# Optimization experiments

Hardware: AMD Instinct MI355X
Metric: run time of the kernel (lower is better)

## Reference

```python
import jax, jax.numpy as jnp
import numpy as np

NHEAD = 16


def setup_inputs() -> dict:
    key = jax.random.key(0)
    ks = jax.random.split(key, 8)
    B, T, C = 2, 1024, 2048
    H, D = NHEAD, C // NHEAD
    P = 1024  # past kv length
    s = 0.02
    return {
        "x": jax.random.normal(ks[0], (B, T, C), jnp.float32),
        "past_k": jax.random.normal(ks[1], (B, H, P, D), jnp.float32),
        "past_v": jax.random.normal(ks[2], (B, H, P, D), jnp.float32),
        "Wk": jax.random.normal(ks[3], (C, C), jnp.float32) * s,
        "Wq": jax.random.normal(ks[4], (C, C), jnp.float32) * s,
        "Wv": jax.random.normal(ks[5], (C, C), jnp.float32) * s,
        "Wp": jax.random.normal(ks[6], (C, C), jnp.float32) * s,
        "bp": jax.random.normal(ks[7], (C,), jnp.float32) * s,
    }


def reference(x, past_k, past_v, Wk, Wq, Wv, Wp, bp):
    B, T, C = x.shape
    H = NHEAD
    D = C // H
    # nn.Linear(W): y = x @ W.T ; split into heads -> [B,H,T,D]
    def proj_heads(W):
        return (x @ W.T).reshape(B, T, H, D).transpose(0, 2, 1, 3)
    q = proj_heads(Wq)
    k_new = proj_heads(Wk)
    v_new = proj_heads(Wv)
    k = jnp.concatenate([past_k, k_new], axis=2)  # [B,H,P+T,D]
    v = jnp.concatenate([past_v, v_new], axis=2)
    past_len = past_k.shape[2]
    total_len = past_len + T
    # causal mask: new-query row i attends to absolute position j <= past_len + i
    q_pos = past_len + jnp.arange(T)[:, None]        # [T,1]
    k_pos = jnp.arange(total_len)[None, :]           # [1,total]
    mask = k_pos <= q_pos                            # [T,total]
    att = jnp.einsum("bhqd,bhkd->bhqk", q, k) * (1.0 / np.sqrt(D).astype(np.float32))
    att = jnp.where(mask[None, None], att, jnp.float32(-jnp.inf))
    att = jax.nn.softmax(att, axis=-1)
    out = jnp.einsum("bhqk,bhkd->bhqd", att, v)
    out = out.transpose(0, 2, 1, 3).reshape(B, T, C)
    out = out @ Wp.T + bp
    return out, k, v
```

## Files before the change

### kernel.cpp

```cpp
#include <hip/hip_runtime.h>
#include <stdint.h>

#define B_ 2
#define T_ 1024
#define C_ 2048
#define H_ 16
#define D_ 128
#define P_ 1024
#define L_ 2048
#define M_ 2048

typedef unsigned short u16;
typedef __attribute__((ext_vector_type(8))) short short8;
typedef __attribute__((ext_vector_type(4))) float f32x4;
typedef __attribute__((ext_vector_type(8))) u16 u16x8;
typedef __attribute__((ext_vector_type(4))) u16 u16x4;

__device__ __forceinline__ u16 f2bf(float x) {
    union { float f; uint32_t u; } c; c.f = x;
    uint32_t u = c.u;
    return (u16)((u + 0x7fffu + ((u >> 16) & 1u)) >> 16);
}

__device__ __forceinline__ void gload_lds16(const void* g, void* l) {
    typedef __attribute__((address_space(1))) const void gvoid;
    typedef __attribute__((address_space(3))) void lvoid;
    __builtin_amdgcn_global_load_lds((gvoid*)g, (lvoid*)l, 16, 0, 0);
}

__global__ __launch_bounds__(256) void convert_bf16_kernel(
        const float* __restrict__ in, u16* __restrict__ out) {
    int i = blockIdx.x * 256 + threadIdx.x;
    const float4* p = (const float4*)in;
    float4 a = p[i * 2], b = p[i * 2 + 1];
    ((u16x8*)out)[i] = u16x8{f2bf(a.x), f2bf(a.y), f2bf(a.z), f2bf(a.w),
                             f2bf(b.x), f2bf(b.y), f2bf(b.z), f2bf(b.w)};
}

__global__ __launch_bounds__(256) void copy_past_kernel(
        const float4* __restrict__ pk, const float4* __restrict__ pv,
        float4* __restrict__ kdst, float4* __restrict__ vdst,
        u16x4* __restrict__ kb) {
    int i = blockIdx.x * 256 + threadIdx.x;
    int bh = i >> 15;
    int rest = i & 32767;
    size_t dst = (size_t)bh * (L_ * D_ / 4) + rest;
    float4 k4 = pk[i], v4 = pv[i];
    kdst[dst] = k4;
    vdst[dst] = v4;
    kb[dst] = u16x4{f2bf(k4.x), f2bf(k4.y), f2bf(k4.z), f2bf(k4.w)};
}

__global__ __launch_bounds__(256) void vT_past_kernel(
        const float* __restrict__ pv, u16* __restrict__ vbT) {
    __shared__ float s[64][65];
    const int tid = threadIdx.x;
    const int bh = blockIdx.x >> 5;
    const int tile = blockIdx.x & 31;
    const int k0 = (tile >> 1) * 64;
    const int d0 = (tile & 1) * 64;
    const float* src = pv + ((size_t)bh * P_ + k0) * D_ + d0;
    {
        int r = tid >> 2, c0 = (tid & 3) * 16;
#pragma unroll
        for (int u = 0; u < 4; ++u) {
            float4 f = *(const float4*)(src + (size_t)r * D_ + c0 + u * 4);
            s[r][c0 + u * 4 + 0] = f.x; s[r][c0 + u * 4 + 1] = f.y;
            s[r][c0 + u * 4 + 2] = f.z; s[r][c0 + u * 4 + 3] = f.w;
        }
    }
    __syncthreads();
    int d = tid >> 2, ck = (tid & 3) * 16;
    u16* dst = vbT + ((size_t)bh * D_ + d0 + d) * L_ + k0 + ck;
    u16x8 o0, o1;
#pragma unroll
    for (int j = 0; j < 8; ++j) o0[j] = f2bf(s[ck + j][d]);
#pragma unroll
    for (int j = 0; j < 8; ++j) o1[j] = f2bf(s[ck + 8 + j][d]);
    *(u16x8*)dst = o0;
    *(u16x8*)(dst + 8) = o1;
}

template <int MODE>
__global__ __launch_bounds__(256) void gemm128(
        const u16* __restrict__ A, const u16* __restrict__ Bw,
        float* __restrict__ outf, u16* __restrict__ outb,
        const float* __restrict__ bias) {
    __shared__ u16 As[128 * 32];
    __shared__ u16 Bs[128 * 32];
    const int tid  = threadIdx.x;
    const int wave = tid >> 6;
    const int lane = tid & 63;
    const int m0 = blockIdx.y * 128;
    const int n0 = blockIdx.x * 128;

    f32x4 acc[4][4];
#pragma unroll
    for (int i = 0; i < 4; ++i)
#pragma unroll
        for (int j = 0; j < 4; ++j) acc[i][j] = f32x4{0.f, 0.f, 0.f, 0.f};

    const int srow = lane >> 2;
    const int scol = (lane & 3) * 8;
    const int q0 = wave * 2, q1 = wave * 2 + 1;
    const u16* A0 = A  + (size_t)(m0 + q0 * 16 + srow) * C_ + scol;
    const u16* A1 = A  + (size_t)(m0 + q1 * 16 + srow) * C_ + scol;
    const u16* B0 = Bw + (size_t)(n0 + q0 * 16 + srow) * C_ + scol;
    const u16* B1 = Bw + (size_t)(n0 + q1 * 16 + srow) * C_ + scol;

    const int frow = lane & 15;
    const int fko  = (lane >> 4) * 8;
    const int wr = (wave >> 1) * 64;
    const int wc = (wave & 1) * 64;

    for (int kt = 0; kt < C_; kt += 32) {
        __syncthreads();
        gload_lds16(A0 + kt, &As[q0 * 512]);
        gload_lds16(A1 + kt, &As[q1 * 512]);
        gload_lds16(B0 + kt, &Bs[q0 * 512]);
        gload_lds16(B1 + kt, &Bs[q1 * 512]);
        __syncthreads();
        short8 af[4], bf[4];
#pragma unroll
        for (int i = 0; i < 4; ++i) {
            af[i] = *(const short8*)&As[(wr + i * 16 + frow) * 32 + fko];
            bf[i] = *(const short8*)&Bs[(wc + i * 16 + frow) * 32 + fko];
        }
#pragma unroll
        for (int mi = 0; mi < 4; ++mi)
#pragma unroll
            for (int ni = 0; ni < 4; ++ni)
                acc[mi][ni] = __builtin_amdgcn_mfma_f32_16x16x32_bf16(
                    af[mi], bf[ni], acc[mi][ni], 0, 0, 0);
    }

    const int ccol = lane & 15;
    const int crb  = (lane >> 4) * 4;
#pragma unroll
    for (int mi = 0; mi < 4; ++mi) {
#pragma unroll
        for (int ni = 0; ni < 4; ++ni) {
            const int gc  = n0 + wc + ni * 16 + ccol;
            const int grb = m0 + wr + mi * 16 + crb;
            if (MODE == 0) {
#pragma unroll
                for (int r = 0; r < 4; ++r)
                    outb[(size_t)(grb + r) * C_ + gc] = f2bf(acc[mi][ni][r]);
            } else if (MODE == 2) {
                const float ba = bias[gc];
#pragma unroll
                for (int r = 0; r < 4; ++r)
                    outf[(size_t)(grb + r) * C_ + gc] = acc[mi][ni][r] + ba;
            } else {
                const int b = grb >> 10, tb = grb & 1023;
                const int h = gc >> 7,  d  = gc & 127;
                const size_t fb = (((size_t)(b * H_ + h)) * L_ + P_ + tb) * D_ + d;
#pragma unroll
                for (int r = 0; r < 4; ++r) outf[fb + (size_t)r * D_] = acc[mi][ni][r];
                if (MODE == 1) {
#pragma unroll
                    for (int r = 0; r < 4; ++r)
                        outb[fb + (size_t)r * D_] = f2bf(acc[mi][ni][r]);
                } else {
                    const size_t tb2 = (((size_t)(b * H_ + h)) * D_ + d) * L_ + P_ + tb;
                    *(u16x4*)&outb[tb2] = u16x4{
                        f2bf(acc[mi][ni][0]), f2bf(acc[mi][ni][1]),
                        f2bf(acc[mi][ni][2]), f2bf(acc[mi][ni][3])};
                }
            }
        }
    }
}

#define NEG_BIG -30000.f
__global__ __launch_bounds__(256) void attn_kernel(
        const u16* __restrict__ Q, const u16* __restrict__ Kb,
        const u16* __restrict__ VT, u16* __restrict__ O) {
    __shared__ u16 Qs[64 * 128];
    __shared__ u16 Ks[64 * 128];
    __shared__ u16 Vs[128 * 64];
    __shared__ u16 Ps[64][72];

    const int tid  = threadIdx.x;
    const int wave = tid >> 6;
    const int lane = tid & 63;
    const int qt = blockIdx.x & 15;
    const int h  = (blockIdx.x >> 4) & 15;
    const int b  = blockIdx.x >> 8;
    const int t0 = qt * 64;

    const u16* Kbase = Kb + (size_t)(b * H_ + h) * L_ * D_;
    const u16* Vbase = VT + (size_t)(b * H_ + h) * D_ * L_;

#pragma unroll
    for (int i = 0; i < 4; ++i) {
        int g   = (wave * 4 + i) * 64 + lane;
        int row = g >> 4, blk = g & 15;
        int sb  = (blk & 8) | ((blk ^ row) & 7);
        gload_lds16(Q + ((size_t)(b * T_ + t0 + row)) * C_ + h * D_ + sb * 8,
                    &Qs[(wave * 4 + i) * 512]);
    }

    const int frow = lane & 15;
    const int quad = lane >> 4;
    const int fko  = quad * 8;
    const int swz  = (frow & 7) << 3;

    f32x4 o_acc[8];
#pragma unroll
    for (int n = 0; n < 8; ++n) o_acc[n] = f32x4{0.f, 0.f, 0.f, 0.f};
    float m_i[4] = {NEG_BIG, NEG_BIG, NEG_BIG, NEG_BIG};
    float l_i[4] = {0.f, 0.f, 0.f, 0.f};
    const float scale = 0.08838834764831845f;

    const int nch = (P_ + t0 + 64) >> 6;

    for (int ch = 0; ch < nch; ++ch) {
        const int j0 = ch * 64;
        __syncthreads();
#pragma unroll
        for (int i = 0; i < 4; ++i) {
            int g = (wave * 4 + i) * 64 + lane;
            {
                int row = g >> 4, blk = g & 15;
                int sb  = (blk & 8) | ((blk ^ row) & 7);
                gload_lds16(Kbase + (size_t)(j0 + row) * D_ + sb * 8,
                            &Ks[(wave * 4 + i) * 512]);
            }
            {
                int d  = g >> 3, cb = g & 7;
                int sb = (cb ^ d) & 7;
                gload_lds16(Vbase + (size_t)d * L_ + j0 + sb * 8,
                            &Vs[(wave * 4 + i) * 512]);
            }
        }
        __syncthreads();

        f32x4 st[4];
#pragma unroll
        for (int j = 0; j < 4; ++j) st[j] = f32x4{0.f, 0.f, 0.f, 0.f};
#pragma unroll
        for (int kt = 0; kt < 4; ++kt) {
            short8 a = *(const short8*)&Qs[(wave * 16 + frow) * 128 +
                                           ((kt * 32 + fko) ^ swz)];
#pragma unroll
            for (int j = 0; j < 4; ++j) {
                short8 kf = *(const short8*)&Ks[(j * 16 + frow) * 128 +
                                                ((kt * 32 + fko) ^ swz)];
                st[j] = __builtin_amdgcn_mfma_f32_16x16x32_bf16(a, kf, st[j], 0, 0, 0);
            }
        }

#pragma unroll
        for (int r = 0; r < 4; ++r) {
            const int t   = t0 + wave * 16 + quad * 4 + r;
            const int lim = P_ + t;
            float sv[4];
            float mx = NEG_BIG;
#pragma unroll
            for (int j = 0; j < 4; ++j) {
                int jg = j0 + j * 16 + frow;
                float s = st[j][r] * scale;
                s = (jg <= lim) ? s : NEG_BIG;
                sv[j] = s;
                mx = fmaxf(mx, s);
            }
#pragma unroll
            for (int sft = 1; sft <= 8; sft <<= 1)
                mx = fmaxf(mx, __shfl_xor(mx, sft, 64));
            float m_new = fmaxf(m_i[r], mx);
            float alpha = __expf(fminf(m_i[r] - m_new, 0.f));
            float rs = 0.f;
#pragma unroll
            for (int j = 0; j < 4; ++j) {
                float p = __expf(fminf(sv[j] - m_new, 0.f));
                p = (sv[j] <= NEG_BIG) ? 0.f : p;
                sv[j] = p;
                rs += p;
            }
#pragma unroll
            for (int sft = 1; sft <= 8; sft <<= 1)
                rs += __shfl_xor(rs, sft, 64);
            l_i[r] = l_i[r] * alpha + rs;
            m_i[r] = m_new;
#pragma unroll
            for (int n = 0; n < 8; ++n) o_acc[n][r] *= alpha;
#pragma unroll
            for (int j = 0; j < 4; ++j)
                Ps[wave * 16 + quad * 4 + r][j * 16 + frow] = f2bf(sv[j]);
        }
        __syncthreads();

#pragma unroll
        for (int kt2 = 0; kt2 < 2; ++kt2) {
            short8 a = *(const short8*)&Ps[wave * 16 + frow][kt2 * 32 + fko];
#pragma unroll
            for (int n = 0; n < 8; ++n) {
                short8 vf = *(const short8*)&Vs[(n * 16 + frow) * 64 +
                                                ((kt2 * 32 + fko) ^ swz)];
                o_acc[n] = __builtin_amdgcn_mfma_f32_16x16x32_bf16(a, vf, o_acc[n], 0, 0, 0);
            }
        }
    }

#pragma unroll
    for (int r = 0; r < 4; ++r) {
        float rl = 1.f / fmaxf(l_i[r], 1e-30f);
        int t = t0 + wave * 16 + quad * 4 + r;
#pragma unroll
        for (int n = 0; n < 8; ++n) {
            float v = o_acc[n][r] * rl;
            O[((size_t)(b * T_ + t)) * C_ + h * D_ + n * 16 + frow] = f2bf(v);
        }
    }
}

extern "C" void kernel_launch(void* const* d_in, const int* in_sizes, int n_in,
                              void* d_out, int out_size, void* d_ws, size_t ws_size,
                              hipStream_t stream) {
    const float* x      = (const float*)d_in[0];
    const float* past_k = (const float*)d_in[1];
    const float* past_v = (const float*)d_in[2];
    const float* Wk     = (const float*)d_in[3];
    const float* Wq     = (const float*)d_in[4];
    const float* Wv     = (const float*)d_in[5];
    const float* Wp     = (const float*)d_in[6];
    const float* bp     = (const float*)d_in[7];

    float* out  = (float*)d_out;
    float* kout = out + 4194304;
    float* vout = kout + 8388608;

    u16* Qst = (u16*)d_out;
    u16* xb  = (u16*)((char*)d_out + (8u << 20));
    u16* Ost = (u16*)d_ws;
    u16* kb  = (u16*)((char*)d_ws + (8u  << 20));
    u16* vbT = (u16*)((char*)d_ws + (24u << 20));
    u16* Wb  = (u16*)((char*)d_ws + (40u << 20));

    copy_past_kernel<<<4096, 256, 0, stream>>>(
        (const float4*)past_k, (const float4*)past_v,
        (float4*)kout, (float4*)vout, (u16x4*)kb);
    vT_past_kernel<<<1024, 256, 0, stream>>>(past_v, vbT);
    convert_bf16_kernel<<<2048, 256, 0, stream>>>(x, xb);

    dim3 g(16, 16);
    convert_bf16_kernel<<<2048, 256, 0, stream>>>(Wk, Wb);
    gemm128<1><<<g, 256, 0, stream>>>(xb, Wb, kout, kb, nullptr);
    convert_bf16_kernel<<<2048, 256, 0, stream>>>(Wv, Wb);
    gemm128<3><<<g, 256, 0, stream>>>(xb, Wb, vout, vbT, nullptr);
    convert_bf16_kernel<<<2048, 256, 0, stream>>>(Wq, Wb);
    gemm128<0><<<g, 256, 0, stream>>>(xb, Wb, nullptr, Qst, nullptr);

    attn_kernel<<<512, 256, 0, stream>>>(Qst, kb, vbT, Ost);

    convert_bf16_kernel<<<2048, 256, 0, stream>>>(Wp, Wb);
    gemm128<2><<<g, 256, 0, stream>>>(Ost, Wb, out, nullptr, bp);
}
```

Before: 476.5 us.

## Fuse QKV conversions and GEMMs, skip masked attention chunks, defer softmax rescale

Merges the four fp32-to-bf16 conversions of x, Wk, Wv and Wq into one launch, and the three projection GEMMs into one wider grid that picks its weight and output by column region. The fused grid is used only when the workspace is large enough, with a fallback split otherwise. In attention, waves whose rows are fully masked for a chunk skip both MFMA phases. Batch 1 reverses its query-tile order to even out the causal load, and s_setprio wraps the MFMA phases. The online softmax skips the rescale when the row max grows by at most 8, which risks reduced exp range or precision.

New measurement: 443.3 us. -7.0%, faster.

```diff
diff --git a/kernel.cpp b/kernel.cpp
--- a/kernel.cpp
+++ b/kernel.cpp
@@ -26,6 +26,21 @@
     typedef __attribute__((address_space(1))) const void gvoid;
     typedef __attribute__((address_space(3))) void lvoid;
     __builtin_amdgcn_global_load_lds((gvoid*)g, (lvoid*)l, 16, 0, 0);
+}
+
+__global__ __launch_bounds__(256) void convert4_kernel(
+        const float* __restrict__ x,  const float* __restrict__ wk,
+        const float* __restrict__ wv, const float* __restrict__ wq,
+        u16* __restrict__ xb, u16* __restrict__ obK,
+        u16* __restrict__ obV, u16* __restrict__ obQ) {
+    const int bid = blockIdx.x;
+    const int r = bid >> 11;
+    const int i = (bid & 2047) * 256 + threadIdx.x;
+    const float* src = (r == 0) ? x : (r == 1) ? wk : (r == 2) ? wv : wq;
+    u16* dst = (r == 0) ? xb : (r == 1) ? obK : (r == 2) ? obV : obQ;
+    float4 a = ((const float4*)src)[i * 2], b = ((const float4*)src)[i * 2 + 1];
+    ((u16x8*)dst)[i] = u16x8{f2bf(a.x), f2bf(a.y), f2bf(a.z), f2bf(a.w),
+                             f2bf(b.x), f2bf(b.y), f2bf(b.z), f2bf(b.w)};
 }
 
 __global__ __launch_bounds__(256) void convert_bf16_kernel(
@@ -81,6 +96,98 @@
     *(u16x8*)(dst + 8) = o1;
 }
 
+__global__ __launch_bounds__(256) void gemm_qkv(
+        const u16* __restrict__ A,
+        const u16* __restrict__ wbK, const u16* __restrict__ wbV,
+        const u16* __restrict__ wbQ,
+        float* __restrict__ kout, float* __restrict__ vout,
+        u16* __restrict__ kb, u16* __restrict__ vbT, u16* __restrict__ Qst) {
+    __shared__ u16 As[128 * 32];
+    __shared__ u16 Bs[128 * 32];
+    const int tid  = threadIdx.x;
+    const int wave = tid >> 6;
+    const int lane = tid & 63;
+    const int m0   = blockIdx.y * 128;
+    const int n0g  = blockIdx.x * 128;
+    const int region = n0g >> 11;
+    const int n0   = n0g & 2047;
+    const u16* Bw = (region == 0) ? wbK : (region == 1) ? wbV : wbQ;
+
+    f32x4 acc[4][4];
+#pragma unroll
+    for (int i = 0; i < 4; ++i)
+#pragma unroll
+        for (int j = 0; j < 4; ++j) acc[i][j] = f32x4{0.f, 0.f, 0.f, 0.f};
+
+    const int srow = lane >> 2;
+    const int scol = (lane & 3) * 8;
+    const int q0 = wave * 2, q1 = wave * 2 + 1;
+    const u16* A0 = A  + (size_t)(m0 + q0 * 16 + srow) * C_ + scol;
+    const u16* A1 = A  + (size_t)(m0 + q1 * 16 + srow) * C_ + scol;
+    const u16* B0 = Bw + (size_t)(n0 + q0 * 16 + srow) * C_ + scol;
+    const u16* B1 = Bw + (size_t)(n0 + q1 * 16 + srow) * C_ + scol;
+
+    const int frow = lane & 15;
+    const int fko  = (lane >> 4) * 8;
+    const int wr = (wave >> 1) * 64;
+    const int wc = (wave & 1) * 64;
+
+    for (int kt = 0; kt < C_; kt += 32) {
+        __syncthreads();
+        gload_lds16(A0 + kt, &As[q0 * 512]);
+        gload_lds16(A1 + kt, &As[q1 * 512]);
+        gload_lds16(B0 + kt, &Bs[q0 * 512]);
+        gload_lds16(B1 + kt, &Bs[q1 * 512]);
+        __syncthreads();
+        short8 af[4], bf[4];
+#pragma unroll
+        for (int i = 0; i < 4; ++i) {
+            af[i] = *(const short8*)&As[(wr + i * 16 + frow) * 32 + fko];
+            bf[i] = *(const short8*)&Bs[(wc + i * 16 + frow) * 32 + fko];
+        }
+#pragma unroll
+        for (int mi = 0; mi < 4; ++mi)
+#pragma unroll
+            for (int ni = 0; ni < 4; ++ni)
+                acc[mi][ni] = __builtin_amdgcn_mfma_f32_16x16x32_bf16(
+                    af[mi], bf[ni], acc[mi][ni], 0, 0, 0);
+    }
+
+    const int ccol = lane & 15;
+    const int crb  = (lane >> 4) * 4;
+#pragma unroll
+    for (int mi = 0; mi < 4; ++mi) {
+#pragma unroll
+        for (int ni = 0; ni < 4; ++ni) {
+            const int gc  = n0 + wc + ni * 16 + ccol;
+            const int grb = m0 + wr + mi * 16 + crb;
+            if (region == 2) {
+#pragma unroll
+                for (int r = 0; r < 4; ++r)
+                    Qst[(size_t)(grb + r) * C_ + gc] = f2bf(acc[mi][ni][r]);
+            } else {
+                const int b = grb >> 10, tb = grb & 1023;
+                const int h = gc >> 7,  d  = gc & 127;
+                const size_t fb = (((size_t)(b * H_ + h)) * L_ + P_ + tb) * D_ + d;
+                if (region == 0) {
+#pragma unroll
+                    for (int r = 0; r < 4; ++r) {
+                        kout[fb + (size_t)r * D_] = acc[mi][ni][r];
+                        kb[fb + (size_t)r * D_]   = f2bf(acc[mi][ni][r]);
+                    }
+                } else {
+#pragma unroll
+                    for (int r = 0; r < 4; ++r) vout[fb + (size_t)r * D_] = acc[mi][ni][r];
+                    const size_t tb2 = (((size_t)(b * H_ + h)) * D_ + d) * L_ + P_ + tb;
+                    *(u16x4*)&vbT[tb2] = u16x4{
+                        f2bf(acc[mi][ni][0]), f2bf(acc[mi][ni][1]),
+                        f2bf(acc[mi][ni][2]), f2bf(acc[mi][ni][3])};
+                }
+            }
+        }
+    }
+}
+
 template <int MODE>
 __global__ __launch_bounds__(256) void gemm128(
         const u16* __restrict__ A, const u16* __restrict__ Bw,
@@ -146,27 +253,11 @@
 #pragma unroll
                 for (int r = 0; r < 4; ++r)
                     outb[(size_t)(grb + r) * C_ + gc] = f2bf(acc[mi][ni][r]);
-            } else if (MODE == 2) {
+            } else {
                 const float ba = bias[gc];
 #pragma unroll
                 for (int r = 0; r < 4; ++r)
                     outf[(size_t)(grb + r) * C_ + gc] = acc[mi][ni][r] + ba;
-            } else {
-                const int b = grb >> 10, tb = grb & 1023;
-                const int h = gc >> 7,  d  = gc & 127;
-                const size_t fb = (((size_t)(b * H_ + h)) * L_ + P_ + tb) * D_ + d;
-#pragma unroll
-                for (int r = 0; r < 4; ++r) outf[fb + (size_t)r * D_] = acc[mi][ni][r];
-                if (MODE == 1) {
-#pragma unroll
-                    for (int r = 0; r < 4; ++r)
-                        outb[fb + (size_t)r * D_] = f2bf(acc[mi][ni][r]);
-                } else {
-                    const size_t tb2 = (((size_t)(b * H_ + h)) * D_ + d) * L_ + P_ + tb;
-                    *(u16x4*)&outb[tb2] = u16x4{
-                        f2bf(acc[mi][ni][0]), f2bf(acc[mi][ni][1]),
-                        f2bf(acc[mi][ni][2]), f2bf(acc[mi][ni][3])};
-                }
             }
         }
     }
@@ -184,9 +275,10 @@
     const int tid  = threadIdx.x;
     const int wave = tid >> 6;
     const int lane = tid & 63;
-    const int qt = blockIdx.x & 15;
+    int       qt = blockIdx.x & 15;
     const int h  = (blockIdx.x >> 4) & 15;
     const int b  = blockIdx.x >> 8;
+    if (b) qt = 15 - qt;
     const int t0 = qt * 64;
 
     const u16* Kbase = Kb + (size_t)(b * H_ + h) * L_ * D_;
@@ -214,6 +306,7 @@
     const float scale = 0.08838834764831845f;
 
     const int nch = (P_ + t0 + 64) >> 6;
+    const int wave_lim = P_ + t0 + wave * 16 + 15;
 
     for (int ch = 0; ch < nch; ++ch) {
         const int j0 = ch * 64;
@@ -236,70 +329,84 @@
         }
         __syncthreads();
 
-        f32x4 st[4];
-#pragma unroll
-        for (int j = 0; j < 4; ++j) st[j] = f32x4{0.f, 0.f, 0.f, 0.f};
-#pragma unroll
-        for (int kt = 0; kt < 4; ++kt) {
-            short8 a = *(const short8*)&Qs[(wave * 16 + frow) * 128 +
-                                           ((kt * 32 + fko) ^ swz)];
-#pragma unroll
-            for (int j = 0; j < 4; ++j) {
-                short8 kf = *(const short8*)&Ks[(j * 16 + frow) * 128 +
-                                                ((kt * 32 + fko) ^ swz)];
-                st[j] = __builtin_amdgcn_mfma_f32_16x16x32_bf16(a, kf, st[j], 0, 0, 0);
-            }
-        }
-
-#pragma unroll
-        for (int r = 0; r < 4; ++r) {
-            const int t   = t0 + wave * 16 + quad * 4 + r;
-            const int lim = P_ + t;
-            float sv[4];
-            float mx = NEG_BIG;
-#pragma unroll
-            for (int j = 0; j < 4; ++j) {
-                int jg = j0 + j * 16 + frow;
-                float s = st[j][r] * scale;
-                s = (jg <= lim) ? s : NEG_BIG;
-                sv[j] = s;
-                mx = fmaxf(mx, s);
-            }
-#pragma unroll
-            for (int sft = 1; sft <= 8; sft <<= 1)
-                mx = fmaxf(mx, __shfl_xor(mx, sft, 64));
-            float m_new = fmaxf(m_i[r], mx);
-            float alpha = __expf(fminf(m_i[r] - m_new, 0.f));
-            float rs = 0.f;
-#pragma unroll
-            for (int j = 0; j < 4; ++j) {
-                float p = __expf(fminf(sv[j] - m_new, 0.f));
-                p = (sv[j] <= NEG_BIG) ? 0.f : p;
-                sv[j] = p;
-                rs += p;
-            }
-#pragma unroll
-            for (int sft = 1; sft <= 8; sft <<= 1)
-                rs += __shfl_xor(rs, sft, 64);
-            l_i[r] = l_i[r] * alpha + rs;
-            m_i[r] = m_new;
-#pragma unroll
-            for (int n = 0; n < 8; ++n) o_acc[n][r] *= alpha;
-#pragma unroll
-            for (int j = 0; j < 4; ++j)
-                Ps[wave * 16 + quad * 4 + r][j * 16 + frow] = f2bf(sv[j]);
-        }
-        __syncthreads();
-
-#pragma unroll
-        for (int kt2 = 0; kt2 < 2; ++kt2) {
-            short8 a = *(const short8*)&Ps[wave * 16 + frow][kt2 * 32 + fko];
-#pragma unroll
-            for (int n = 0; n < 8; ++n) {
-                short8 vf = *(const short8*)&Vs[(n * 16 + frow) * 64 +
-                                                ((kt2 * 32 + fko) ^ swz)];
-                o_acc[n] = __builtin_amdgcn_mfma_f32_16x16x32_bf16(a, vf, o_acc[n], 0, 0, 0);
-            }
+        const bool active = (j0 <= wave_lim);
+
+        if (active) {
+            f32x4 st[4];
+#pragma unroll
+            for (int j = 0; j < 4; ++j) st[j] = f32x4{0.f, 0.f, 0.f, 0.f};
+            __builtin_amdgcn_s_setprio(1);
+#pragma unroll
+            for (int kt = 0; kt < 4; ++kt) {
+                short8 a = *(const short8*)&Qs[(wave * 16 + frow) * 128 +
+                                               ((kt * 32 + fko) ^ swz)];
+#pragma unroll
+                for (int j = 0; j < 4; ++j) {
+                    short8 kf = *(const short8*)&Ks[(j * 16 + frow) * 128 +
+                                                    ((kt * 32 + fko) ^ swz)];
+                    st[j] = __builtin_amdgcn_mfma_f32_16x16x32_bf16(a, kf, st[j], 0, 0, 0);
+                }
+            }
+            __builtin_amdgcn_s_setprio(0);
+
+#pragma unroll
+            for (int r = 0; r < 4; ++r) {
+                const int t   = t0 + wave * 16 + quad * 4 + r;
+                const int lim = P_ + t;
+                float sv[4];
+                float mx = NEG_BIG;
+#pragma unroll
+                for (int j = 0; j < 4; ++j) {
+                    int jg = j0 + j * 16 + frow;
+                    float s = st[j][r] * scale;
+                    s = (jg <= lim) ? s : NEG_BIG;
+                    sv[j] = s;
+                    mx = fmaxf(mx, s);
+                }
+#pragma unroll
+                for (int sft = 1; sft <= 8; sft <<= 1)
+                    mx = fmaxf(mx, __shfl_xor(mx, sft, 64));
+                const bool defer = (mx <= m_i[r] + 8.f);
+                const float m_new = defer ? m_i[r] : mx;
+                float rs = 0.f;
+#pragma unroll
+                for (int j = 0; j < 4; ++j) {
+                    float p = (sv[j] <= NEG_BIG) ? 0.f : __expf(sv[j] - m_new);
+                    sv[j] = p;
+                    rs += p;
+                }
+#pragma unroll
+                for (int sft = 1; sft <= 8; sft <<= 1)
+                    rs += __shfl_xor(rs, sft, 64);
+                if (defer) {
+                    l_i[r] += rs;
+                } else {
+                    float alpha = __expf(fminf(m_i[r] - m_new, 0.f));
+                    l_i[r] = l_i[r] * alpha + rs;
+                    m_i[r] = m_new;
+#pragma unroll
+                    for (int n = 0; n < 8; ++n) o_acc[n][r] *= alpha;
+                }
+#pragma unroll
+                for (int j = 0; j < 4; ++j)
+                    Ps[wave * 16 + quad * 4 + r][j * 16 + frow] = f2bf(sv[j]);
+            }
+        }
+        __syncthreads();
+
+        if (active) {
+            __builtin_amdgcn_s_setprio(1);
+#pragma unroll
+            for (int kt2 = 0; kt2 < 2; ++kt2) {
+                short8 a = *(const short8*)&Ps[wave * 16 + frow][kt2 * 32 + fko];
+#pragma unroll
+                for (int n = 0; n < 8; ++n) {
+                    short8 vf = *(const short8*)&Vs[(n * 16 + frow) * 64 +
+                                                    ((kt2 * 32 + fko) ^ swz)];
+                    o_acc[n] = __builtin_amdgcn_mfma_f32_16x16x32_bf16(a, vf, o_acc[n], 0, 0, 0);
+                }
+            }
+            __builtin_amdgcn_s_setprio(0);
         }
     }
 
@@ -333,27 +440,36 @@
 
     u16* Qst = (u16*)d_out;
     u16* xb  = (u16*)((char*)d_out + (8u << 20));
-    u16* Ost = (u16*)d_ws;
-    u16* kb  = (u16*)((char*)d_ws + (8u  << 20));
-    u16* vbT = (u16*)((char*)d_ws + (24u << 20));
-    u16* Wb  = (u16*)((char*)d_ws + (40u << 20));
+    u16* OstWq = (u16*)d_ws;
+    u16* kb    = (u16*)((char*)d_ws + (8u  << 20));
+    u16* vbT   = (u16*)((char*)d_ws + (24u << 20));
+    u16* wbKP  = (u16*)((char*)d_ws + (40u << 20));
+    const bool fused = ws_size >= (size_t)(56u << 20);
+    u16* wbV = fused ? (u16*)((char*)d_ws + (48u << 20))
+                     : Qst;
+
+    convert4_kernel<<<8192, 256, 0, stream>>>(x, Wk, Wv, Wq, xb, wbKP, wbV, OstWq);
 
     copy_past_kernel<<<4096, 256, 0, stream>>>(
         (const float4*)past_k, (const float4*)past_v,
         (float4*)kout, (float4*)vout, (u16x4*)kb);
     vT_past_kernel<<<1024, 256, 0, stream>>>(past_v, vbT);
-    convert_bf16_kernel<<<2048, 256, 0, stream>>>(x, xb);
-
-    dim3 g(16, 16);
-    convert_bf16_kernel<<<2048, 256, 0, stream>>>(Wk, Wb);
-    gemm128<1><<<g, 256, 0, stream>>>(xb, Wb, kout, kb, nullptr);
-    convert_bf16_kernel<<<2048, 256, 0, stream>>>(Wv, Wb);
-    gemm128<3><<<g, 256, 0, stream>>>(xb, Wb, vout, vbT, nullptr);
-    convert_bf16_kernel<<<2048, 256, 0, stream>>>(Wq, Wb);
-    gemm128<0><<<g, 256, 0, stream>>>(xb, Wb, nullptr, Qst, nullptr);
-
-    attn_kernel<<<512, 256, 0, stream>>>(Qst, kb, vbT, Ost);
-
-    convert_bf16_kernel<<<2048, 256, 0, stream>>>(Wp, Wb);
-    gemm128<2><<<g, 256, 0, stream>>>(Ost, Wb, out, nullptr, bp);
-}
+
+    if (fused) {
+        dim3 g(48, 16);
+        gemm_qkv<<<g, 256, 0, stream>>>(xb, wbKP, wbV, OstWq,
+                                        kout, vout, kb, vbT, Qst);
+    } else {
+        dim3 gkv(32, 16);
+        gemm_qkv<<<gkv, 256, 0, stream>>>(xb, wbKP, wbV, OstWq,
+                                          kout, vout, kb, vbT, Qst);
+        dim3 gq(16, 16);
+        gemm128<0><<<gq, 256, 0, stream>>>(xb, OstWq, nullptr, Qst, nullptr);
+    }
+
+    attn_kernel<<<512, 256, 0, stream>>>(Qst, kb, vbT, OstWq);
+
+    convert_bf16_kernel<<<2048, 256, 0, stream>>>(Wp, wbKP);
+    dim3 gp(16, 16);
+    gemm128<2><<<gp, 256, 0, stream>>>(OstWq, wbKP, out, nullptr, bp);
+}
```
